# Optimization experiments

Hardware: AMD Instinct MI355X
Metric: run time of the kernel (lower is better)

Reference implementation:

```python
import jax, jax.numpy as jnp
import numpy as np

B, N, DIM, HEADS = 8, 512, 512, 16
MAX_DIST, NG = 128, 32
RBF_STOP = 20.0
EPS = 1e-5


def _ln(x, g, b):
    m = jnp.mean(x, axis=-1, keepdims=True)
    v = jnp.mean((x - m) ** 2, axis=-1, keepdims=True)
    return (x - m) * jax.lax.rsqrt(v + EPS) * g + b


def setup_inputs() -> dict:
    key = jax.random.key(0)
    ks = jax.random.split(key, 12)
    d = DIM
    s = 0.02
    return {
        "x": jax.random.normal(ks[0], (B * N, d), jnp.float32),
        "dist_matrix": jax.random.randint(ks[1], (B, N, N), 0, MAX_DIST, jnp.int32),
        "dist_3d": jax.random.uniform(ks[2], (B, N, N), jnp.float32) * RBF_STOP,
        "norm1_g": jnp.ones((d,), jnp.float32),
        "norm1_b": jnp.zeros((d,), jnp.float32),
        "in_proj_w": jax.random.normal(ks[3], (3 * d, d), jnp.float32) * s,
        "in_proj_b": jnp.zeros((3 * d,), jnp.float32),
        "out_proj_w": jax.random.normal(ks[4], (d, d), jnp.float32) * s,
        "out_proj_b": jnp.zeros((d,), jnp.float32),
        "dist_emb": jax.random.normal(ks[5], (MAX_DIST, HEADS), jnp.float32) * s,
        "rbf_w": jax.random.normal(ks[6], (HEADS, NG), jnp.float32) * s,
        "rbf_b": jnp.zeros((HEADS,), jnp.float32),
        "norm2_g": jnp.ones((d,), jnp.float32),
        "norm2_b": jnp.zeros((d,), jnp.float32),
        "ffn_w1": jax.random.normal(ks[7], (4 * d, d), jnp.float32) * s,
        "ffn_b1": jnp.zeros((4 * d,), jnp.float32),
        "ffn_w2": jax.random.normal(ks[8], (d, 4 * d), jnp.float32) * s,
        "ffn_b2": jnp.zeros((d,), jnp.float32),
        "batch": jnp.repeat(jnp.arange(B, dtype=jnp.int32), N),
    }


def reference(x, dist_matrix, dist_3d, norm1_g, norm1_b, in_proj_w, in_proj_b,
              out_proj_w, out_proj_b, dist_emb, rbf_w, rbf_b, norm2_g, norm2_b,
              ffn_w1, ffn_b1, ffn_w2, ffn_b2, batch):
    b, n = dist_matrix.shape[0], dist_matrix.shape[1]
    d = x.shape[-1]
    dh = d // HEADS
    # equal-size graphs -> to_dense_batch is a reshape, mask all-true
    xd = x.reshape(b, n, d)

    # additive attention bias: shortest-path-distance embedding + RBF projection
    dc = jnp.clip(dist_matrix, 0, MAX_DIST - 1)
    bias_spd = dist_emb[dc]                                  # [b, n, n, H]
    offset = jnp.linspace(0.0, RBF_STOP, NG, dtype=jnp.float32)
    coeff = -0.5 / (RBF_STOP / (NG - 1)) ** 2
    rbf = jnp.exp(coeff * (dist_3d[..., None] - offset) ** 2)  # [b, n, n, NG]
    bias_3d = rbf @ rbf_w.T + rbf_b                          # [b, n, n, H]
    bias = jnp.transpose(bias_spd + bias_3d, (0, 3, 1, 2))   # [b, H, n, n]

    # multi-head attention (pre-norm residual, as in source)
    h = _ln(xd, norm1_g, norm1_b)
    qkv = h @ in_proj_w.T + in_proj_b
    q, k, v = jnp.split(qkv, 3, axis=-1)
    q = q.reshape(b, n, HEADS, dh).transpose(0, 2, 1, 3)
    k = k.reshape(b, n, HEADS, dh).transpose(0, 2, 1, 3)
    v = v.reshape(b, n, HEADS, dh).transpose(0, 2, 1, 3)
    scores = jnp.einsum('bhqd,bhkd->bhqk', q, k) / jnp.sqrt(jnp.float32(dh)) + bias
    attn = jax.nn.softmax(scores, axis=-1)
    ctx = jnp.einsum('bhqk,bhkd->bhqd', attn, v)
    ctx = ctx.transpose(0, 2, 1, 3).reshape(b, n, d)
    attn_out = ctx @ out_proj_w.T + out_proj_b
    h = h + attn_out

    # FFN (dropout inactive at eval)
    h2 = _ln(h, norm2_g, norm2_b)
    ff = jax.nn.gelu(h2 @ ffn_w1.T + ffn_b1, approximate=False) @ ffn_w2.T + ffn_b2
    h = h + ff
    return h.reshape(b * n, d)
```

## Files before the change

### kernel.cpp

```cpp
#include <hip/hip_runtime.h>
#include <hip/hip_bf16.h>
#include <math.h>

#define BB 8
#define NN 512
#define DD 512
#define NH 16
#define DH 32
#define TD 1536
#define NG 32
#define MAXD 128

typedef __attribute__((ext_vector_type(8))) short bf16x8;
typedef __attribute__((ext_vector_type(4))) float f32x4;
typedef __attribute__((ext_vector_type(2))) unsigned int u32x2;
typedef __attribute__((ext_vector_type(4))) unsigned int u32x4;

__device__ inline short f2bf(float x) {
    __hip_bfloat16 h = __float2bfloat16(x);
    return *reinterpret_cast<short*>(&h);
}
__device__ inline float bf2f(short x) {
    union { unsigned u; float f; } c;
    c.u = ((unsigned)(unsigned short)x) << 16;
    return c.f;
}
__device__ inline unsigned cvt_pk_bf16(float lo, float hi) {
    unsigned r;
    asm("v_cvt_pk_bf16_f32 %0, %1, %2" : "=v"(r) : "v"(lo), "v"(hi));
    return r;
}
__device__ inline float exp2fast(float x) {
    float r;
    asm("v_exp_f32 %0, %1" : "=v"(r) : "v"(x));
    return r;
}

__device__ inline void gld_lds16(const void* g, void* l) {
    __builtin_amdgcn_global_load_lds(
        (const __attribute__((address_space(1))) unsigned int*)g,
        (__attribute__((address_space(3))) unsigned int*)l, 16, 0, 0);
}

__global__ __launch_bounds__(256) void prep(
    const float* __restrict__ x, const float* __restrict__ n1g,
    const float* __restrict__ n1b, short* __restrict__ h_bf,
    const float* __restrict__ s0, const float* __restrict__ s1,
    const float* __restrict__ s2, const float* __restrict__ s3,
    short* __restrict__ d0, short* __restrict__ d1,
    short* __restrict__ d2, short* __restrict__ d3,
    const float* __restrict__ rbfw, const float* __restrict__ rbfb,
    short* __restrict__ Tg,
    int n0, int n1, int n2, int n3) {
    const int tid = threadIdx.x;
    if (blockIdx.x < 4096) {
        const int row = blockIdx.x;
        const int wave = tid >> 6, lane = tid & 63;
        const float* xr = x + (size_t)row * DD;
        const float2 v01 = *(const float2*)(xr + 2 * tid);
        float s = v01.x + v01.y, q = v01.x * v01.x + v01.y * v01.y;
#pragma unroll
        for (int m = 1; m < 64; m <<= 1) { s += __shfl_xor(s, m); q += __shfl_xor(q, m); }
        __shared__ float ps[8];
        if (lane == 0) { ps[wave] = s; ps[wave + 4] = q; }
        __syncthreads();
        s = ps[0] + ps[1] + ps[2] + ps[3];
        q = ps[4] + ps[5] + ps[6] + ps[7];
        const float mean = s * (1.0f / DD);
        const float var  = q * (1.0f / DD) - mean * mean;
        const float rs   = rsqrtf(var + 1e-5f);
        const float2 g2 = *(const float2*)(n1g + 2 * tid);
        const float2 b2 = *(const float2*)(n1b + 2 * tid);
        const float o0 = (v01.x - mean) * rs * g2.x + b2.x;
        const float o1 = (v01.y - mean) * rs * g2.y + b2.y;
        *(unsigned*)&h_bf[(size_t)row * DD + 2 * tid] = cvt_pk_bf16(o0, o1);
        return;
    }
    const int bx = blockIdx.x - 4096;
    const int y = bx >> 9, xb = bx & 511;
    if (y == 4) {
        if (xb != 0) return;
        const float STEP  = 20.0f / 31.0f;
        const float COEFF = -0.5f / (STEP * STEP);
        for (int idx = tid; idx < 194 * 16; idx += 256) {
            const int i = idx >> 4, h = idx & 15;
            const float xx = fminf((float)i, 192.0f) * (20.0f / 192.0f);
            float acc = rbfb[h];
#pragma unroll
            for (int g = 0; g < NG; g++) {
                const float t = xx - (float)g * STEP;
                acc += __expf(COEFF * t * t) * rbfw[h * NG + g];
            }
            Tg[idx] = f2bf(acc * 1.44269504088896f);
        }
        return;
    }
    const float* s; short* d; int n;
    switch (y) {
        case 0: s = s0; d = d0; n = n0; break;
        case 1: s = s1; d = d1; n = n1; break;
        case 2: s = s2; d = d2; n = n2; break;
        default: s = s3; d = d3; n = n3; break;
    }
    const int i = (xb * 256 + tid) * 8;
    if (i >= n) return;
    const float4 a = *(const float4*)(s + i);
    const float4 b = *(const float4*)(s + i + 4);
    u32x4 o;
    o[0] = cvt_pk_bf16(a.x, a.y);
    o[1] = cvt_pk_bf16(a.z, a.w);
    o[2] = cvt_pk_bf16(b.x, b.y);
    o[3] = cvt_pk_bf16(b.z, b.w);
    *(u32x4*)(d + i) = o;
}

template <int TM, bool GELU, int RESMODE, bool OUTBF>
__global__ __launch_bounds__(256) void gemm_bf16(
    const short* __restrict__ A, const short* __restrict__ Bw,
    const float* __restrict__ bias, const void* __restrict__ res,
    void* __restrict__ Cout, int M, int Nout, int K) {
    const int MI = (TM >= 32) ? TM / 32 : 1;
    const int bm = blockIdx.y * TM;
    const int bn = blockIdx.x * 128;
    const int tid  = threadIdx.x;
    const int wave = tid >> 6;
    const int lane = tid & 63;
    const int l16  = lane & 15;
    const int quad = lane >> 4;
    const int wr = (wave >> 1) * (TM / 2);
    const int wc = (wave & 1) * 64;

    __shared__ short As[2][TM * 32];
    __shared__ short Bs[2][128 * 32];

    f32x4 acc[MI][4];
#pragma unroll
    for (int i = 0; i < MI; i++)
#pragma unroll
        for (int j = 0; j < 4; j++) acc[i][j] = (f32x4){0.f, 0.f, 0.f, 0.f};

    auto stage = [&](int buf, int k0) {
        const short* Ab = A + (size_t)bm * K + k0;
        const short* Bb = Bw + (size_t)bn * K + k0;
        if (TM >= 64) {
#pragma unroll
            for (int j = 0; j < TM / 64; j++) {
                const int idx = j * 256 + tid;
                gld_lds16(Ab + (size_t)(idx >> 2) * K + (idx & 3) * 8,
                          &As[buf][(size_t)(j * 256 + wave * 64) * 8]);
            }
        } else {
            if (tid < 128)
                gld_lds16(Ab + (size_t)(tid >> 2) * K + (tid & 3) * 8,
                          &As[buf][(size_t)(wave * 64) * 8]);
        }
#pragma unroll
        for (int j = 0; j < 2; j++) {
            const int idx = j * 256 + tid;
            gld_lds16(Bb + (size_t)(idx >> 2) * K + (idx & 3) * 8,
                      &Bs[buf][(size_t)(j * 256 + wave * 64) * 8]);
        }
    };
    auto compute = [&](int buf) {
        bf16x8 af[MI], bfr[4];
#pragma unroll
        for (int i = 0; i < MI; i++)
            af[i] = *(const bf16x8*)&As[buf][(wr + i * 16 + l16) * 32 + quad * 8];
#pragma unroll
        for (int j = 0; j < 4; j++)
            bfr[j] = *(const bf16x8*)&Bs[buf][(wc + j * 16 + l16) * 32 + quad * 8];
#pragma unroll
        for (int i = 0; i < MI; i++)
#pragma unroll
            for (int j = 0; j < 4; j++)
                acc[i][j] = __builtin_amdgcn_mfma_f32_16x16x32_bf16(bfr[j], af[i], acc[i][j], 0, 0, 0);
    };

    stage(0, 0);
    __syncthreads();
    int cur = 0;
    for (int k0 = 32; k0 < K; k0 += 32) {
        stage(cur ^ 1, k0);
        compute(cur);
        __syncthreads();
        cur ^= 1;
    }
    compute(cur);

#pragma unroll
    for (int i = 0; i < MI; i++) {
        const int row = bm + wr + i * 16 + l16;
#pragma unroll
        for (int j = 0; j < 4; j++) {
            const int col = bn + wc + j * 16 + quad * 4;
            const float4 b4 = *(const float4*)&bias[col];
            float v[4] = {acc[i][j][0] + b4.x, acc[i][j][1] + b4.y,
                          acc[i][j][2] + b4.z, acc[i][j][3] + b4.w};
            if (GELU) {
#pragma unroll
                for (int r = 0; r < 4; r++)
                    v[r] = 0.5f * v[r] * (1.0f + erff(v[r] * 0.70710678118654752f));
            }
            if (RESMODE == 1) {
                const float4 r4 = *(const float4*)&((const float*)res)[(size_t)row * Nout + col];
                v[0] += r4.x; v[1] += r4.y; v[2] += r4.z; v[3] += r4.w;
            }
            if (RESMODE == 2) {
                const short4 r4 = *(const short4*)&((const short*)res)[(size_t)row * Nout + col];
                v[0] += bf2f(r4.x); v[1] += bf2f(r4.y); v[2] += bf2f(r4.z); v[3] += bf2f(r4.w);
            }
            if (OUTBF) {
                u32x2 o;
                o[0] = cvt_pk_bf16(v[0], v[1]);
                o[1] = cvt_pk_bf16(v[2], v[3]);
                *(u32x2*)&((short*)Cout)[(size_t)row * Nout + col] = o;
            } else {
                *(float4*)&((float*)Cout)[(size_t)row * Nout + col] =
                    (float4){v[0], v[1], v[2], v[3]};
            }
        }
    }
}

__global__ __launch_bounds__(512, 2) void attn_fused(
    const short* __restrict__ qkv,
    const int* __restrict__ dist,
    const float* __restrict__ dist3d,
    const float* __restrict__ demb,
    const short* __restrict__ Tg,
    const short* __restrict__ wo,
    const float* __restrict__ bo,
    const short* __restrict__ hb,
    const float* __restrict__ g2v,
    const float* __restrict__ b2v,
    float* __restrict__ hres,
    short* __restrict__ h2) {
    const int blk  = blockIdx.x;
    const int b    = blk & 7;
    const int q0   = (blk >> 3) * 16;
    const int tid  = threadIdx.x;
    const int wave = tid >> 6;
    const int lane = tid & 63;
    const int l16  = lane & 15;
    const int quad = lane >> 4;
    const int hh0  = wave * 2;

    __shared__ short Vc[2][NH * 1024];
    __shared__ short Pb[16 * 512];
    __shared__ short Tt[194 * 18];
    __shared__ short Db[128 * 18];
    __shared__ unsigned short Pk[512 * 16];
    __shared__ float St[2][16][8];

    for (int i = tid; i < 194 * 16; i += 512) Tt[(i >> 4) * 18 + (i & 15)] = Tg[i];
    for (int i = tid; i < 128 * 16; i += 512)
        Db[(i >> 4) * 18 + (i & 15)] = f2bf(demb[i] * 1.44269504088896f);
    {
        const size_t rb = ((size_t)(b * NN) + q0) * NN;
#pragma unroll
        for (int q = 0; q < 16; q++) {
            const size_t off = rb + (size_t)q * NN + tid;
            int dc = dist[off];
            dc = min(max(dc, 0), MAXD - 1);
            int ii = (int)(dist3d[off] * 9.6f + 0.5f);
            ii = min(ii, 192);
            Pk[tid * 16 + q] = (unsigned short)(dc | (ii << 8));
        }
    }

    const float scale = 0.17677669529663687f * 1.44269504088896f;
    bf16x8 qf[2];
#pragma unroll
    for (int h = 0; h < 2; h++)
        qf[h] = *(const bf16x8*)(qkv + (size_t)(b * NN + q0 + l16) * TD + (hh0 + h) * DH + quad * 8);

    f32x4 O[2][2];
    float lsum[2][4];
#pragma unroll
    for (int h = 0; h < 2; h++) {
#pragma unroll
        for (int tt = 0; tt < 2; tt++) O[h][tt] = (f32x4){0.f, 0.f, 0.f, 0.f};
#pragma unroll
        for (int r = 0; r < 4; r++) lsum[h][r] = 0.f;
    }

    __syncthreads();

    const int sk = lane >> 2;
    const int sc = lane & 3;

    auto stageV = [&](int buf, int c) {
        const size_t rowb = (size_t)(b * NN + c * 32 + sk) * TD + 2 * DD + sc * 8;
#pragma unroll
        for (int h = 0; h < 2; h++) {
            short* dst = &Vc[buf][(hh0 + h) * 1024];
            gld_lds16(qkv + rowb + (hh0 + h) * DH, dst);
            gld_lds16(qkv + rowb + (size_t)16 * TD + (hh0 + h) * DH, dst + 512);
        }
    };
    auto loadK = [&](int c, bf16x8 (*kd)[2]) {
#pragma unroll
        for (int h = 0; h < 2; h++) {
            const short* base =
                qkv + (size_t)(b * NN + c * 32 + l16) * TD + DD + (hh0 + h) * DH + quad * 8;
            kd[h][0] = *(const bf16x8*)base;
            kd[h][1] = *(const bf16x8*)(base + 16 * TD);
        }
    };

    bf16x8 kf[2][2], kfn[2][2];
    stageV(0, 0);
    loadK(0, kf);
    int cur = 0;

    for (int c = 0; c < 16; c++) {
        asm volatile("" ::: "memory");
        __builtin_amdgcn_s_waitcnt(0x0F70);
        asm volatile("" ::: "memory");

        u32x2 vraw[2][4];
#pragma unroll
        for (int h = 0; h < 2; h++) {
            const unsigned va =
                (unsigned)(uintptr_t)&Vc[cur][(hh0 + h) * 1024 + quad * 128 + l16];
            asm volatile("ds_read_b64_tr_b16 %0, %1 offset:0"    : "=v"(vraw[h][0]) : "v"(va));
            asm volatile("ds_read_b64_tr_b16 %0, %1 offset:128"  : "=v"(vraw[h][1]) : "v"(va));
            asm volatile("ds_read_b64_tr_b16 %0, %1 offset:1024" : "=v"(vraw[h][2]) : "v"(va));
            asm volatile("ds_read_b64_tr_b16 %0, %1 offset:1152" : "=v"(vraw[h][3]) : "v"(va));
        }

        if (c + 1 < 16) {
            stageV(cur ^ 1, c + 1);
            loadK(c + 1, kfn);
        }

#pragma unroll
        for (int half = 0; half < 2; half++) {
            const ushort4 pk4 =
                *(const ushort4*)&Pk[(unsigned)((c * 32 + half * 16 + l16) * 16 + quad * 4)];
            const unsigned short pe[4] = {pk4.x, pk4.y, pk4.z, pk4.w};
            float bb[2][4];
#pragma unroll
            for (int r = 0; r < 4; r++) {
                const unsigned u  = pe[r];
                const unsigned dc = u & 0xFFu;
                const unsigned ii = u >> 8;
                const unsigned du = *(const unsigned*)&Db[dc * 18 + hh0];
                const unsigned tu = *(const unsigned*)&Tt[ii * 18 + hh0];
                union { unsigned x; float f; } a0, a1, b0, b1;
                a0.x = du << 16; a1.x = du & 0xFFFF0000u;
                b0.x = tu << 16; b1.x = tu & 0xFFFF0000u;
                bb[0][r] = a0.f + b0.f;
                bb[1][r] = a1.f + b1.f;
            }
#pragma unroll
            for (int h = 0; h < 2; h++) {
                f32x4 s = __builtin_amdgcn_mfma_f32_16x16x32_bf16(
                    qf[h], kf[h][half], (f32x4){0.f, 0.f, 0.f, 0.f}, 0, 0, 0);
                float pv[4];
#pragma unroll
                for (int r = 0; r < 4; r++) {
                    float sv = s[r] * scale + bb[h][r];
                    sv = fminf(sv, 28.853901f);
                    pv[r] = exp2fast(sv);
                    lsum[h][r] += pv[r];
                }
                u32x2 w;
                w[0] = cvt_pk_bf16(pv[0], pv[1]);
                w[1] = cvt_pk_bf16(pv[2], pv[3]);
                *(u32x2*)&Pb[(wave * 2 + h) * 512 + (half * 16 + l16) * 16 + quad * 4] = w;
            }
        }

        asm volatile("" ::: "memory");
        asm volatile("s_waitcnt lgkmcnt(0)" ::: "memory");
        __builtin_amdgcn_sched_barrier(0);

        u32x2 praw[2][2];
#pragma unroll
        for (int h = 0; h < 2; h++) {
            const unsigned pa =
                (unsigned)(uintptr_t)&Pb[(wave * 2 + h) * 512 + quad * 64 + l16];
            asm volatile("ds_read_b64_tr_b16 %0, %1 offset:0"   : "=v"(praw[h][0]) : "v"(pa));
            asm volatile("ds_read_b64_tr_b16 %0, %1 offset:512" : "=v"(praw[h][1]) : "v"(pa));
        }
        asm volatile("s_waitcnt lgkmcnt(0)" ::: "memory");
        __builtin_amdgcn_sched_barrier(0);

        __builtin_amdgcn_s_setprio(1);
#pragma unroll
        for (int h = 0; h < 2; h++) {
            union { u32x4 u; bf16x8 s; } pf, v0, v1;
            pf.u = (u32x4){praw[h][0][0], praw[h][0][1], praw[h][1][0], praw[h][1][1]};
#pragma unroll
            for (int r = 0; r < 4; r++) {
                v0.u[r] = __builtin_amdgcn_perm(vraw[h][r][1], vraw[h][r][0], 0x05040100u);
                v1.u[r] = __builtin_amdgcn_perm(vraw[h][r][1], vraw[h][r][0], 0x07060302u);
            }
            O[h][0] = __builtin_amdgcn_mfma_f32_16x16x32_bf16(pf.s, v0.s, O[h][0], 0, 0, 0);
            O[h][1] = __builtin_amdgcn_mfma_f32_16x16x32_bf16(pf.s, v1.s, O[h][1], 0, 0, 0);
        }
        __builtin_amdgcn_s_setprio(0);

#pragma unroll
        for (int h = 0; h < 2; h++) { kf[h][0] = kfn[h][0]; kf[h][1] = kfn[h][1]; }
        cur ^= 1;
    }

#pragma unroll
    for (int h = 0; h < 2; h++) {
#pragma unroll
        for (int m = 1; m < 16; m <<= 1)
#pragma unroll
            for (int r = 0; r < 4; r++) lsum[h][r] += __shfl_xor(lsum[h][r], m);
        float rl[4];
#pragma unroll
        for (int r = 0; r < 4; r++) rl[r] = 1.0f / lsum[h][r];
#pragma unroll
        for (int tt = 0; tt < 2; tt++) {
            const int col = (hh0 + h) * DH + tt * 16 + l16;
            u32x2 w;
            w[0] = cvt_pk_bf16(O[h][tt][0] * rl[0], O[h][tt][1] * rl[1]);
            w[1] = cvt_pk_bf16(O[h][tt][2] * rl[2], O[h][tt][3] * rl[3]);
            *(u32x2*)&Pb[col * 16 + quad * 4] = w;
        }
    }
    __syncthreads();

    f32x4 a2[4];
#pragma unroll
    for (int j = 0; j < 4; j++) a2[j] = (f32x4){0.f, 0.f, 0.f, 0.f};
    const int wcol = wave * 64;
    for (int k0 = 0; k0 < DD; k0 += 32) {
        u32x2 p0, p1;
        const unsigned pa = (unsigned)(uintptr_t)&Pb[k0 * 16 + quad * 64 + l16];
        asm volatile("ds_read_b64_tr_b16 %0, %1 offset:0"   : "=v"(p0) : "v"(pa));
        asm volatile("ds_read_b64_tr_b16 %0, %1 offset:512" : "=v"(p1) : "v"(pa));
        u32x2 blo[4], bhi[4];
#pragma unroll
        for (int j = 0; j < 4; j++) {
            const short* wb = wo + (size_t)(wcol + j * 16 + l16) * DD + k0 + quad * 4;
            blo[j] = *(const u32x2*)wb;
            bhi[j] = *(const u32x2*)(wb + 16);
        }
        asm volatile("s_waitcnt lgkmcnt(0)" ::: "memory");
        __builtin_amdgcn_sched_barrier(0);
        union { u32x4 u; bf16x8 s; } af;
        af.u = (u32x4){p0[0], p0[1], p1[0], p1[1]};
#pragma unroll
        for (int j = 0; j < 4; j++) {
            union { u32x4 u; bf16x8 s; } bw;
            bw.u = (u32x4){blo[j][0], blo[j][1], bhi[j][0], bhi[j][1]};
            a2[j] = __builtin_amdgcn_mfma_f32_16x16x32_bf16(af.s, bw.s, a2[j], 0, 0, 0);
        }
    }

    const int rowg = b * NN + q0;
    float vv[4][4];
    float sp[4] = {0.f, 0.f, 0.f, 0.f}, qp[4] = {0.f, 0.f, 0.f, 0.f};
#pragma unroll
    for (int j = 0; j < 4; j++) {
        const int col = wcol + j * 16 + l16;
        const float bc = bo[col];
#pragma unroll
        for (int r = 0; r < 4; r++) {
            const size_t row = (size_t)rowg + quad * 4 + r;
            const float v = a2[j][r] + bc + bf2f(hb[row * DD + col]);
            hres[row * DD + col] = v;
            vv[j][r] = v;
            sp[r] += v; qp[r] += v * v;
        }
    }
#pragma unroll
    for (int m = 1; m < 16; m <<= 1)
#pragma unroll
        for (int r = 0; r < 4; r++) {
            sp[r] += __shfl_xor(sp[r], m);
            qp[r] += __shfl_xor(qp[r], m);
        }
    if (l16 == 0) {
#pragma unroll
        for (int r = 0; r < 4; r++) {
            St[0][quad * 4 + r][wave] = sp[r];
            St[1][quad * 4 + r][wave] = qp[r];
        }
    }
    __syncthreads();
    float mean[4], rsd[4];
#pragma unroll
    for (int r = 0; r < 4; r++) {
        const int rr = quad * 4 + r;
        float s = 0.f, q = 0.f;
#pragma unroll
        for (int w = 0; w < 8; w++) { s += St[0][rr][w]; q += St[1][rr][w]; }
        mean[r] = s * (1.0f / DD);
        rsd[r]  = rsqrtf(q * (1.0f / DD) - mean[r] * mean[r] + 1e-5f);
    }
#pragma unroll
    for (int j = 0; j < 4; j++) {
        const int col = wcol + j * 16 + l16;
        const float gc = g2v[col], bc2 = b2v[col];
#pragma unroll
        for (int r = 0; r < 4; r++) {
            const size_t row = (size_t)rowg + quad * 4 + r;
            h2[row * DD + col] = f2bf((vv[j][r] - mean[r]) * rsd[r] * gc + bc2);
        }
    }
}

extern "C" void kernel_launch(void* const* d_in, const int* in_sizes, int n_in,
                              void* d_out, int out_size, void* d_ws, size_t ws_size,
                              hipStream_t stream) {
    const float* x      = (const float*)d_in[0];
    const int*   dist   = (const int*)d_in[1];
    const float* dist3d = (const float*)d_in[2];
    const float* n1g    = (const float*)d_in[3];
    const float* n1b    = (const float*)d_in[4];
    const float* win    = (const float*)d_in[5];
    const float* bin    = (const float*)d_in[6];
    const float* wo     = (const float*)d_in[7];
    const float* bo     = (const float*)d_in[8];
    const float* demb   = (const float*)d_in[9];
    const float* rbfw   = (const float*)d_in[10];
    const float* rbfb   = (const float*)d_in[11];
    const float* n2g    = (const float*)d_in[12];
    const float* n2b    = (const float*)d_in[13];
    const float* w1     = (const float*)d_in[14];
    const float* b1     = (const float*)d_in[15];
    const float* w2     = (const float*)d_in[16];
    const float* b2     = (const float*)d_in[17];

    char* p = (char*)d_ws;
    short* h_bf   = (short*)p; p += (size_t)4096 * 512 * 2;
    short* qkv_bf = (short*)p; p += (size_t)4096 * 1536 * 2;
    float* hres   = (float*)p; p += (size_t)4096 * 512 * 4;
    short* h2_bf  = (short*)p; p += (size_t)4096 * 512 * 2;
    short* win_bf = (short*)p; p += (size_t)1536 * 512 * 2;
    short* wo_bf  = (short*)p; p += (size_t)512 * 512 * 2;
    short* w1_bf  = (short*)p; p += (size_t)2048 * 512 * 2;
    short* w2_bf  = (short*)p; p += (size_t)512 * 2048 * 2;
    short* Tg     = (short*)p; p += (size_t)8192;
    short* mid_bf = (short*)p; p += (size_t)4096 * 2048 * 2;

    const int M = BB * NN;

    prep<<<4096 + 2560, 256, 0, stream>>>(
        x, n1g, n1b, h_bf,
        win, wo, w1, w2, win_bf, wo_bf, w1_bf, w2_bf, rbfw, rbfb, Tg,
        1536 * 512, 512 * 512, 2048 * 512, 512 * 2048);
    gemm_bf16<128, false, 0, true><<<dim3(12, 32), 256, 0, stream>>>(
        h_bf, win_bf, bin, nullptr, qkv_bf, M, TD, DD);
    attn_fused<<<256, 512, 0, stream>>>(
        qkv_bf, dist, dist3d, demb, Tg, wo_bf, bo, h_bf, n2g, n2b, hres, h2_bf);
    gemm_bf16<128, true, 0, true><<<dim3(16, 32), 256, 0, stream>>>(
        h2_bf, w1_bf, b1, nullptr, mid_bf, M, 2048, DD);
    gemm_bf16<32, false, 1, false><<<dim3(4, 128), 256, 0, stream>>>(
        mid_bf, w2_bf, b2, hres, (float*)d_out, M, DD, 2048);
}
```

Baseline: 258.6 us.

## Single-buffer V tile for higher occupancy and prefetch out-proj weights

Drops the double-buffered V LDS tile to a single buffer and raises the launch bound to 4 blocks per CU, aiming for more resident waves to hide latency. Adds a wait on the V transposed reads before restaging the same buffer. The out-projection loop is unrolled with weight loads prefetched one step ahead in a register double buffer, and the residual loads are hoisted before the GEMM. This risks register pressure or spills from the tighter launch bound, and loses the overlap of V staging with compute.

```diff
diff --git a/kernel.cpp b/kernel.cpp
--- a/kernel.cpp
+++ b/kernel.cpp
@@ -222,7 +222,7 @@
     }
 }
 
-__global__ __launch_bounds__(512, 2) void attn_fused(
+__global__ __launch_bounds__(512, 4) void attn_fused(
     const short* __restrict__ qkv,
     const int* __restrict__ dist,
     const float* __restrict__ dist3d,
@@ -245,7 +245,7 @@
     const int quad = lane >> 4;
     const int hh0  = wave * 2;
 
-    __shared__ short Vc[2][NH * 1024];
+    __shared__ short Vc[NH * 1024];
     __shared__ short Pb[16 * 512];
     __shared__ short Tt[194 * 18];
     __shared__ short Db[128 * 18];
@@ -289,11 +289,11 @@
     const int sk = lane >> 2;
     const int sc = lane & 3;
 
-    auto stageV = [&](int buf, int c) {
+    auto stageV = [&](int c) {
         const size_t rowb = (size_t)(b * NN + c * 32 + sk) * TD + 2 * DD + sc * 8;
 #pragma unroll
         for (int h = 0; h < 2; h++) {
-            short* dst = &Vc[buf][(hh0 + h) * 1024];
+            short* dst = &Vc[(hh0 + h) * 1024];
             gld_lds16(qkv + rowb + (hh0 + h) * DH, dst);
             gld_lds16(qkv + rowb + (size_t)16 * TD + (hh0 + h) * DH, dst + 512);
         }
@@ -309,9 +309,8 @@
     };
 
     bf16x8 kf[2][2], kfn[2][2];
-    stageV(0, 0);
+    stageV(0);
     loadK(0, kf);
-    int cur = 0;
 
     for (int c = 0; c < 16; c++) {
         asm volatile("" ::: "memory");
@@ -322,15 +321,17 @@
 #pragma unroll
         for (int h = 0; h < 2; h++) {
             const unsigned va =
-                (unsigned)(uintptr_t)&Vc[cur][(hh0 + h) * 1024 + quad * 128 + l16];
+                (unsigned)(uintptr_t)&Vc[(hh0 + h) * 1024 + quad * 128 + l16];
             asm volatile("ds_read_b64_tr_b16 %0, %1 offset:0"    : "=v"(vraw[h][0]) : "v"(va));
             asm volatile("ds_read_b64_tr_b16 %0, %1 offset:128"  : "=v"(vraw[h][1]) : "v"(va));
             asm volatile("ds_read_b64_tr_b16 %0, %1 offset:1024" : "=v"(vraw[h][2]) : "v"(va));
             asm volatile("ds_read_b64_tr_b16 %0, %1 offset:1152" : "=v"(vraw[h][3]) : "v"(va));
         }
+        asm volatile("s_waitcnt lgkmcnt(0)" ::: "memory");
+        __builtin_amdgcn_sched_barrier(0);
 
         if (c + 1 < 16) {
-            stageV(cur ^ 1, c + 1);
+            stageV(c + 1);
             loadK(c + 1, kfn);
         }
 
@@ -404,7 +405,6 @@
 
 #pragma unroll
         for (int h = 0; h < 2; h++) { kf[h][0] = kfn[h][0]; kf[h][1] = kfn[h][1]; }
-        cur ^= 1;
     }
 
 #pragma unroll
@@ -427,21 +427,40 @@
     }
     __syncthreads();
 
+    const int rowg = b * NN + q0;
+    const int wcol = wave * 64;
+    short hbr[4][4];
+#pragma unroll
+    for (int j = 0; j < 4; j++)
+#pragma unroll
+        for (int r = 0; r < 4; r++)
+            hbr[j][r] = hb[((size_t)rowg + quad * 4 + r) * DD + wcol + j * 16 + l16];
+
     f32x4 a2[4];
 #pragma unroll
     for (int j = 0; j < 4; j++) a2[j] = (f32x4){0.f, 0.f, 0.f, 0.f};
-    const int wcol = wave * 64;
-    for (int k0 = 0; k0 < DD; k0 += 32) {
+    u32x2 blo[2][4], bhi[2][4];
+#pragma unroll
+    for (int j = 0; j < 4; j++) {
+        const short* wb = wo + (size_t)(wcol + j * 16 + l16) * DD + quad * 4;
+        blo[0][j] = *(const u32x2*)wb;
+        bhi[0][j] = *(const u32x2*)(wb + 16);
+    }
+#pragma unroll
+    for (int kk = 0; kk < 16; kk++) {
+        const int k0 = kk * 32;
         u32x2 p0, p1;
         const unsigned pa = (unsigned)(uintptr_t)&Pb[k0 * 16 + quad * 64 + l16];
         asm volatile("ds_read_b64_tr_b16 %0, %1 offset:0"   : "=v"(p0) : "v"(pa));
         asm volatile("ds_read_b64_tr_b16 %0, %1 offset:512" : "=v"(p1) : "v"(pa));
-        u32x2 blo[4], bhi[4];
-#pragma unroll
-        for (int j = 0; j < 4; j++) {
-            const short* wb = wo + (size_t)(wcol + j * 16 + l16) * DD + k0 + quad * 4;
-            blo[j] = *(const u32x2*)wb;
-            bhi[j] = *(const u32x2*)(wb + 16);
+        if (kk + 1 < 16) {
+#pragma unroll
+            for (int j = 0; j < 4; j++) {
+                const short* wb =
+                    wo + (size_t)(wcol + j * 16 + l16) * DD + (k0 + 32) + quad * 4;
+                blo[(kk + 1) & 1][j] = *(const u32x2*)wb;
+                bhi[(kk + 1) & 1][j] = *(const u32x2*)(wb + 16);
+            }
         }
         asm volatile("s_waitcnt lgkmcnt(0)" ::: "memory");
         __builtin_amdgcn_sched_barrier(0);
@@ -450,12 +469,12 @@
 #pragma unroll
         for (int j = 0; j < 4; j++) {
             union { u32x4 u; bf16x8 s; } bw;
-            bw.u = (u32x4){blo[j][0], blo[j][1], bhi[j][0], bhi[j][1]};
+            bw.u = (u32x4){blo[kk & 1][j][0], blo[kk & 1][j][1],
+                           bhi[kk & 1][j][0], bhi[kk & 1][j][1]};
             a2[j] = __builtin_amdgcn_mfma_f32_16x16x32_bf16(af.s, bw.s, a2[j], 0, 0, 0);
         }
     }
 
-    const int rowg = b * NN + q0;
     float vv[4][4];
     float sp[4] = {0.f, 0.f, 0.f, 0.f}, qp[4] = {0.f, 0.f, 0.f, 0.f};
 #pragma unroll
@@ -465,7 +484,7 @@
 #pragma unroll
         for (int r = 0; r < 4; r++) {
             const size_t row = (size_t)rowg + quad * 4 + r;
-            const float v = a2[j][r] + bc + bf2f(hb[row * DD + col]);
+            const float v = a2[j][r] + bc + bf2f(hbr[j][r]);
             hres[row * DD + col] = v;
             vv[j][r] = v;
             sp[r] += v; qp[r] += v * v;
```

Result: no change. 260.2 us (+0.6%).
